# Performance work log

Measured on AMD Instinct MI355X. Metric: run time of the kernel, lower is better.

Reference implementation:

```python
import jax, jax.numpy as jnp
import numpy as np

# LocallyConnected3D: unshared 3D conv, channels_last, valid padding, stride 1,
# linear activation, bias. Implementations 2 and 3 in the original both compute
# out[b,x,y,z,f] = sum_{i,j,k,c} in[b, x+i, y+j, z+k, c] * W[x,y,z,i,j,k,c,f] + bias[x,y,z,f]

B, X, Y, Z, CIN = 8, 32, 32, 16, 8
K = 3            # kernel_size per spatial dim
F = 16           # filters
OX, OY, OZ = X - K + 1, Y - K + 1, Z - K + 1  # 30, 30, 14 (valid, stride 1)


def setup_inputs() -> dict:
    key = jax.random.key(0)
    k1, k2 = jax.random.split(key, 2)
    inputs = jax.random.normal(k1, (B, X, Y, Z, CIN), dtype=jnp.float32)
    # glorot_uniform over the per-location receptive field
    fan_in = K * K * K * CIN
    limit = float(np.sqrt(6.0 / (fan_in + F)))
    kernel = jax.random.uniform(k2, (OX, OY, OZ, K, K, K, CIN, F),
                                dtype=jnp.float32, minval=-limit, maxval=limit)
    bias = jnp.zeros((OX, OY, OZ, F), dtype=jnp.float32)
    return {"inputs": inputs, "kernel": kernel, "bias": bias}


def _extract_patches(x):
    # (B, OX, OY, OZ, K, K, K, CIN); stride 1 valid -> plain shifted slices.
    slices = [x[:, i:i + OX, j:j + OY, k:k + OZ, :]
              for i in range(K) for j in range(K) for k in range(K)]
    p = jnp.stack(slices, axis=4)                # (B, OX, OY, OZ, K^3, CIN)
    return p.reshape(B, OX, OY, OZ, K, K, K, CIN)


def reference(inputs, kernel, bias):
    patches = _extract_patches(inputs)
    out = jnp.einsum('bxyzijkc,xyzijkcf->bxyzf', patches, kernel)
    return out + bias
```

## Files before the change

kernel.cpp:

```cpp
#include <hip/hip_runtime.h>

#define B_   8
#define OXD  30
#define OYD  30
#define OZD  14
#define NLOC (OXD*OYD*OZD)
#define CIN  8
#define F_   16
#define T_   216
#define WPL  (T_*F_)

__global__ __launch_bounds__(128)
void lc3d_kernel(const float* __restrict__ in, const float* __restrict__ wgt,
                 const float* __restrict__ bias, float* __restrict__ out) {
    __shared__ float patch[B_ * T_];
    __shared__ float red[2 * 128];
    float4* patch4 = reinterpret_cast<float4*>(patch);

    const int loc = blockIdx.x;
    const int ox  = loc / (OYD * OZD);
    const int rem = loc - ox * (OYD * OZD);
    const int oy  = rem / OZD;
    const int oz  = rem - oy * OZD;
    const int tid = threadIdx.x;

    const int fq = tid & 3;
    const int tg = tid >> 2;
    const float* wloc = wgt + (size_t)loc * WPL;

    const float bi = bias[loc * F_ + (tid & 15)];

    float4 w[7];
    #pragma unroll
    for (int it = 0; it < 6; ++it)
        w[it] = *reinterpret_cast<const float4*>(wloc + (tg + 32 * it) * F_ + fq * 4);
    w[6] = make_float4(0.f, 0.f, 0.f, 0.f);
    if (tg < 24)
        w[6] = *reinterpret_cast<const float4*>(wloc + (tg + 192) * F_ + fq * 4);

    const float4* in4 = reinterpret_cast<const float4*>(in);
    #pragma unroll
    for (int r = 0; r < 4; ++r) {
        int idx = tid + 128 * r;
        if (r < 3 || idx < 432) {
            int seg = idx / 6;
            int off = idx - seg * 6;
            int b   = seg / 9;
            int ij  = seg - b * 9;
            int i   = ij / 3;
            int j   = ij - i * 3;
            int g4  = (((b * 32 + ox + i) * 32 + (oy + j)) * 16 + oz) * 2 + off;
            patch4[idx] = in4[g4];
        }
    }
    __syncthreads();

    float a[32];
    #pragma unroll
    for (int e = 0; e < 32; ++e) a[e] = 0.f;

    #pragma unroll
    for (int it = 0; it < 7; ++it) {
        const int t  = tg + 32 * it;
        const int tc = (t < T_) ? t : 0;
        const float4 ww = w[it];
        #pragma unroll
        for (int b = 0; b < B_; ++b) {
            const float p = patch[b * T_ + tc];
            a[b * 4 + 0] += p * ww.x;
            a[b * 4 + 1] += p * ww.y;
            a[b * 4 + 2] += p * ww.z;
            a[b * 4 + 3] += p * ww.w;
        }
    }

#define RSTEP(m, k)                                         \
    {                                                       \
        const bool hi = (tid & (m)) != 0;                   \
        _Pragma("unroll")                                   \
        for (int e = 0; e < (k); ++e) {                     \
            float v = hi ? a[e] : a[e + (k)];               \
            float r = __shfl_xor(v, (m), 64);               \
            a[e] = (hi ? a[e + (k)] : a[e]) + r;            \
        }                                                   \
    }
    RSTEP(4, 16)
    RSTEP(8, 8)
    RSTEP(16, 4)
    RSTEP(32, 2)
#undef RSTEP

    const int eg = ((tid & 4) << 2) | (tid & 8) | ((tid & 16) >> 2) | ((tid & 32) >> 4);
    const int wv = tid >> 6;
    red[wv * 128 + (eg + 0) * 4 + fq] = a[0];
    red[wv * 128 + (eg + 1) * 4 + fq] = a[1];
    __syncthreads();

    {
        const int b   = tid >> 4;
        const int f   = tid & 15;
        const int fq2 = f >> 2;
        const int fi  = f & 3;
        const int e2  = (b * 4 + fi) * 4 + fq2;
        const float s = bi + red[e2] + red[128 + e2];
        out[((size_t)b * NLOC + loc) * F_ + f] = s;
    }
}

extern "C" void kernel_launch(void* const* d_in, const int* in_sizes, int n_in,
                              void* d_out, int out_size, void* d_ws, size_t ws_size,
                              hipStream_t stream) {
    const float* in   = (const float*)d_in[0];
    const float* wgt  = (const float*)d_in[1];
    const float* bias = (const float*)d_in[2];
    float* out = (float*)d_out;
    lc3d_kernel<<<NLOC, 128, 0, stream>>>(in, wgt, bias, out);
}
```

Before: 36.64 us.

## Process two adjacent z locations per block to share input patch loads

```diff
diff --git a/kernel.cpp b/kernel.cpp
--- a/kernel.cpp
+++ b/kernel.cpp
@@ -1,109 +1,122 @@
 #include <hip/hip_runtime.h>
 
-#define B_   8
-#define OXD  30
-#define OYD  30
-#define OZD  14
-#define NLOC (OXD*OYD*OZD)
-#define CIN  8
-#define F_   16
-#define T_   216
-#define WPL  (T_*F_)
+#define B_    8
+#define OXD   30
+#define OYD   30
+#define OZD   14
+#define NLOC  (OXD*OYD*OZD)
+#define F_    16
+#define T_    216
+#define WPL   (T_*F_)
+#define OZH   (OZD/2)
+#define NBLK  (OXD*OYD*OZH)
 
-__global__ __launch_bounds__(128)
+__global__ __launch_bounds__(128, 4)
 void lc3d_kernel(const float* __restrict__ in, const float* __restrict__ wgt,
                  const float* __restrict__ bias, float* __restrict__ out) {
-    __shared__ float patch[B_ * T_];
-    __shared__ float red[2 * 128];
-    float4* patch4 = reinterpret_cast<float4*>(patch);
+    __shared__ float patch[B_ * 9 * 32];
+    __shared__ float red[2][2 * 128];
 
-    const int loc = blockIdx.x;
-    const int ox  = loc / (OYD * OZD);
-    const int rem = loc - ox * (OYD * OZD);
-    const int oy  = rem / OZD;
-    const int oz  = rem - oy * OZD;
+    const int blk = blockIdx.x;
+    const int ox  = blk / (OYD * OZH);
+    const int rem = blk - ox * (OYD * OZH);
+    const int oy  = rem / OZH;
+    const int ozh = rem - oy * OZH;
+    const int oz0 = 2 * ozh;
+    const int loc0 = (ox * OYD + oy) * OZD + oz0;
+
     const int tid = threadIdx.x;
+    const int fq  = tid & 3;
+    const int tg  = tid >> 2;
+    const float* wloc = wgt + (size_t)loc0 * WPL;
 
-    const int fq = tid & 3;
-    const int tg = tid >> 2;
-    const float* wloc = wgt + (size_t)loc * WPL;
+    const float bi0 = bias[(size_t)loc0 * F_ + (tid & 15)];
+    const float bi1 = bias[(size_t)(loc0 + 1) * F_ + (tid & 15)];
 
-    const float bi = bias[loc * F_ + (tid & 15)];
+    float4 w[14];
+    #pragma unroll
+    for (int l = 0; l < 2; ++l) {
+        #pragma unroll
+        for (int it = 0; it < 6; ++it)
+            w[l * 7 + it] = *reinterpret_cast<const float4*>(
+                wloc + l * WPL + (tg + 32 * it) * F_ + fq * 4);
+        w[l * 7 + 6] = make_float4(0.f, 0.f, 0.f, 0.f);
+        if (tg < 24)
+            w[l * 7 + 6] = *reinterpret_cast<const float4*>(
+                wloc + l * WPL + (tg + 192) * F_ + fq * 4);
+    }
 
-    float4 w[7];
-    #pragma unroll
-    for (int it = 0; it < 6; ++it)
-        w[it] = *reinterpret_cast<const float4*>(wloc + (tg + 32 * it) * F_ + fq * 4);
-    w[6] = make_float4(0.f, 0.f, 0.f, 0.f);
-    if (tg < 24)
-        w[6] = *reinterpret_cast<const float4*>(wloc + (tg + 192) * F_ + fq * 4);
-
-    const float4* in4 = reinterpret_cast<const float4*>(in);
-    #pragma unroll
-    for (int r = 0; r < 4; ++r) {
-        int idx = tid + 128 * r;
-        if (r < 3 || idx < 432) {
-            int seg = idx / 6;
-            int off = idx - seg * 6;
-            int b   = seg / 9;
-            int ij  = seg - b * 9;
-            int i   = ij / 3;
-            int j   = ij - i * 3;
-            int g4  = (((b * 32 + ox + i) * 32 + (oy + j)) * 16 + oz) * 2 + off;
-            patch4[idx] = in4[g4];
+    {
+        const float4* in4 = reinterpret_cast<const float4*>(in);
+        float4* patch4 = reinterpret_cast<float4*>(patch);
+        #pragma unroll
+        for (int r = 0; r < 5; ++r) {
+            int idx = tid + 128 * r;
+            if (r < 4 || tid < 64) {
+                int seg = idx >> 3;
+                int off = idx & 7;
+                int b   = seg / 9;
+                int ij  = seg - b * 9;
+                int i   = ij / 3;
+                int j   = ij - i * 3;
+                int g4  = (((b * 32 + ox + i) * 32 + (oy + j)) * 16 + oz0) * 2 + off;
+                patch4[idx] = in4[g4];
+            }
         }
     }
     __syncthreads();
 
-    float a[32];
     #pragma unroll
-    for (int e = 0; e < 32; ++e) a[e] = 0.f;
+    for (int l = 0; l < 2; ++l) {
+        float a[32];
+        #pragma unroll
+        for (int e = 0; e < 32; ++e) a[e] = 0.f;
 
-    #pragma unroll
-    for (int it = 0; it < 7; ++it) {
-        const int t  = tg + 32 * it;
-        const int tc = (t < T_) ? t : 0;
-        const float4 ww = w[it];
         #pragma unroll
-        for (int b = 0; b < B_; ++b) {
-            const float p = patch[b * T_ + tc];
-            a[b * 4 + 0] += p * ww.x;
-            a[b * 4 + 1] += p * ww.y;
-            a[b * 4 + 2] += p * ww.z;
-            a[b * 4 + 3] += p * ww.w;
+        for (int it = 0; it < 7; ++it) {
+            const int t  = tg + 32 * it;
+            const int tc = (t < T_) ? t : 0;
+            const int vi = tc + (tc / 24) * 8 + l * 8;
+            const float4 ww = w[l * 7 + it];
+            #pragma unroll
+            for (int b = 0; b < B_; ++b) {
+                const float p = patch[b * 288 + vi];
+                a[b * 4 + 0] += p * ww.x;
+                a[b * 4 + 1] += p * ww.y;
+                a[b * 4 + 2] += p * ww.z;
+                a[b * 4 + 3] += p * ww.w;
+            }
         }
-    }
 
 #define RSTEP(m, k)                                         \
-    {                                                       \
-        const bool hi = (tid & (m)) != 0;                   \
-        _Pragma("unroll")                                   \
-        for (int e = 0; e < (k); ++e) {                     \
-            float v = hi ? a[e] : a[e + (k)];               \
-            float r = __shfl_xor(v, (m), 64);               \
-            a[e] = (hi ? a[e + (k)] : a[e]) + r;            \
-        }                                                   \
-    }
-    RSTEP(4, 16)
-    RSTEP(8, 8)
-    RSTEP(16, 4)
-    RSTEP(32, 2)
+        {                                                   \
+            const bool hi = (tid & (m)) != 0;               \
+            _Pragma("unroll")                               \
+            for (int e = 0; e < (k); ++e) {                 \
+                float v = hi ? a[e] : a[e + (k)];           \
+                float r = __shfl_xor(v, (m), 64);           \
+                a[e] = (hi ? a[e + (k)] : a[e]) + r;        \
+            }                                               \
+        }
+        RSTEP(4, 16)
+        RSTEP(8, 8)
+        RSTEP(16, 4)
+        RSTEP(32, 2)
 #undef RSTEP
 
-    const int eg = ((tid & 4) << 2) | (tid & 8) | ((tid & 16) >> 2) | ((tid & 32) >> 4);
-    const int wv = tid >> 6;
-    red[wv * 128 + (eg + 0) * 4 + fq] = a[0];
-    red[wv * 128 + (eg + 1) * 4 + fq] = a[1];
-    __syncthreads();
+        const int eg = ((tid & 4) << 2) | (tid & 8) | ((tid & 16) >> 2) | ((tid & 32) >> 4);
+        const int wv = tid >> 6;
+        red[l][wv * 128 + (eg + 0) * 4 + fq] = a[0];
+        red[l][wv * 128 + (eg + 1) * 4 + fq] = a[1];
+        __syncthreads();
 
-    {
-        const int b   = tid >> 4;
-        const int f   = tid & 15;
-        const int fq2 = f >> 2;
-        const int fi  = f & 3;
-        const int e2  = (b * 4 + fi) * 4 + fq2;
-        const float s = bi + red[e2] + red[128 + e2];
-        out[((size_t)b * NLOC + loc) * F_ + f] = s;
+        {
+            const int b   = tid >> 4;
+            const int f   = tid & 15;
+            const int e2  = ((b * 4 + (f & 3)) * 4) + (f >> 2);
+            const float s = (l == 0 ? bi0 : bi1) + red[l][e2] + red[l][128 + e2];
+            out[((size_t)b * NLOC + loc0 + l) * F_ + f] = s;
+        }
     }
 }
 
@@ -114,5 +127,5 @@
     const float* wgt  = (const float*)d_in[1];
     const float* bias = (const float*)d_in[2];
     float* out = (float*)d_out;
-    lc3d_kernel<<<NLOC, 128, 0, stream>>>(in, wgt, bias, out);
+    lc3d_kernel<<<NBLK, 128, 0, stream>>>(in, wgt, bias, out);
 }
```

Result: slower. 38.70 us (+5.6%).
